# Performance work log

Hardware: AMD Instinct MI355X
Metric: run time of the kernel (lower is better)

Reference implementation:

```python
import jax, jax.numpy as jnp
import numpy as np
import math

LMAX = 3
NUM_LAYERS = 2
MUL = 32
AVG_NEIGH = 16.0
CUTOFF = 2.5
P_ENV = 6
N_RB = 8

# ---------- real Clebsch-Gordan (Wigner 3j) coefficients ----------

def _su2_cg(j1, j2, j3, m1, m2, m3):
    if m1 + m2 != m3:
        return 0.0
    f = math.factorial
    pref = math.sqrt((2 * j3 + 1) * f(j1 + j2 - j3) * f(j1 - j2 + j3) * f(-j1 + j2 + j3) / f(j1 + j2 + j3 + 1)
                     * f(j3 + m3) * f(j3 - m3) * f(j1 - m1) * f(j1 + m1) * f(j2 - m2) * f(j2 + m2))
    s = 0.0
    kmin = max(0, j2 - j3 - m1, j1 - j3 + m2)
    kmax = min(j1 + j2 - j3, j1 - m1, j2 + m2)
    for k in range(kmin, kmax + 1):
        s += (-1.0) ** k / (f(k) * f(j1 + j2 - j3 - k) * f(j1 - m1 - k) * f(j2 + m2 - k)
                            * f(j3 - j2 + m1 + k) * f(j3 - j1 - m2 + k))
    return pref * s

def _q_real_to_complex(l):
    q = np.zeros((2 * l + 1, 2 * l + 1), dtype=np.complex128)
    for m in range(-l, 0):
        q[l + m, l + abs(m)] = 1 / np.sqrt(2)
        q[l + m, l - abs(m)] = -1j / np.sqrt(2)
    q[l, l] = 1.0
    for m in range(1, l + 1):
        q[l + m, l + abs(m)] = (-1) ** m / np.sqrt(2)
        q[l + m, l - abs(m)] = 1j * (-1) ** m / np.sqrt(2)
    return (-1j) ** l * q

def _real_cg(l1, l2, l3):
    C = np.zeros((2 * l1 + 1, 2 * l2 + 1, 2 * l3 + 1), dtype=np.complex128)
    for m1 in range(-l1, l1 + 1):
        for m2 in range(-l2, l2 + 1):
            m3 = m1 + m2
            if abs(m3) <= l3:
                C[l1 + m1, l2 + m2, l3 + m3] = _su2_cg(l1, l2, l3, m1, m2, m3)
    Q1, Q2, Q3 = _q_real_to_complex(l1), _q_real_to_complex(l2), _q_real_to_complex(l3)
    C = np.einsum('ia,jb,kc,abc->ijk', Q1, Q2, np.conj(Q3), C)
    Cr, Ci = np.real(C), np.imag(C)
    C = Cr if np.linalg.norm(Cr) >= np.linalg.norm(Ci) else Ci
    return (C / np.linalg.norm(C)).astype(np.float32)  # unit-norm invariant coupling tensor

W3J = {}
for _l1 in range(LMAX + 1):
    for _l2 in range(LMAX + 1):
        for _l3 in range(LMAX + 1):
            if abs(_l1 - _l2) <= _l3 <= _l1 + _l2:
                W3J[(_l1, _l2, _l3)] = jnp.asarray(_real_cg(_l1, _l2, _l3))

# ---------- spherical harmonics (component normalization, l=0..3) ----------

def _sh(u):
    x, y, z = u[:, 0], u[:, 1], u[:, 2]
    s3, s5, s15 = math.sqrt(3.0), math.sqrt(5.0), math.sqrt(15.0)
    sh0 = jnp.ones_like(x)[:, None]
    sh1 = s3 * jnp.stack([y, z, x], -1)
    sh2 = jnp.stack([s15 * x * y, s15 * y * z, 0.5 * s5 * (3 * z * z - 1.0),
                     s15 * x * z, 0.5 * s15 * (x * x - y * y)], -1)
    c1, c2, c3, c4 = math.sqrt(35.0 / 8.0), math.sqrt(105.0), math.sqrt(21.0 / 8.0), 0.5 * math.sqrt(7.0)
    sh3 = jnp.stack([c1 * y * (3 * x * x - y * y), c2 * x * y * z, c3 * y * (5 * z * z - 1.0),
                     c4 * z * (5 * z * z - 3.0), c3 * x * (5 * z * z - 1.0),
                     0.5 * c2 * z * (x * x - y * y), c1 * x * (x * x - 3 * y * y)], -1)
    return [sh0, sh1, sh2, sh3]

def _mlp(x, Ws):
    # e3nn-style MLP: no biases, 1/sqrt(fan_in) normalization, silu, linear last layer
    for i, W in enumerate(Ws):
        x = x @ (W / jnp.sqrt(1.0 * W.shape[0]))
        if i + 1 < len(Ws):
            x = jax.nn.silu(x)
    return x

def _envelope(x):
    p = P_ENV
    e = (1.0 - 0.5 * (p + 1) * (p + 2) * x ** p + p * (p + 2) * x ** (p + 1)
         - 0.5 * p * (p + 1) * x ** (p + 2))
    return jnp.where(x < 1.0, e, 0.0)

def _forward(node_attrs, vectors, we0, we1, winit, wenv, wlat0, wlat1, wmix, wout, senders, receivers):
    N = node_attrs.shape[0]
    E = vectors.shape[0]
    d = jnp.linalg.norm(vectors, axis=-1)                      # [E]
    uvec = vectors / (d[:, None] + 1e-9)                       # unit edge vectors
    dc = d / CUTOFF                                            # normalized distance in [0, inf)
    freqs = np.pi * np.arange(1, N_RB + 1, dtype=np.float32)
    rb = math.sqrt(2.0) * jnp.sin(dc[:, None] * freqs) / (dc[:, None] + 1e-9)  # [E, 8] Bessel basis
    cut = _envelope(dc)[:, None]                               # [E, 1] polynomial cutoff u(d, p)
    # two-body embedding: radial basis + sender/receiver species
    x = jnp.concatenate([rb, node_attrs[senders], node_attrs[receivers]], axis=-1)
    x = _mlp(x, [we0, we1]) * cut                              # [E, H]
    Y = _sh(uvec)                                              # list of [E, 2l+1]
    wi = (x @ (winit / jnp.sqrt(1.0 * winit.shape[0]))).reshape(E, LMAX + 1, MUL)
    V = [wi[:, l, :, None] * Y[l][:, None, :] for l in range(LMAX + 1)]  # [E, MUL, 2l+1]
    for layer in range(NUM_LAYERS):
        w = x @ (wenv[layer] / jnp.sqrt(1.0 * wenv.shape[1]))  # [E, MUL] env weights
        env = []
        for l in range(LMAX + 1):
            # environment embedding: scatter weighted SH onto nodes, gather back onto edges
            node_env = jax.ops.segment_sum(w[:, :, None] * Y[l][:, None, :], receivers, num_segments=N)
            env.append(node_env[senders] / jnp.sqrt(AVG_NEIGH))
        # equivariant CG tensor product env (x) V -> T, per output l3
        T = []
        for l3 in range(LMAX + 1):
            acc = None
            n = 0
            for l1 in range(LMAX + 1):
                for l2 in range(LMAX + 1):
                    if (l1, l2, l3) in W3J:
                        t = jnp.einsum('ijk,emi,emj->emk', W3J[(l1, l2, l3)], env[l1], V[l2])
                        acc = t if acc is None else acc + t
                        n += 1
            T.append(acc / np.sqrt(n))
        # scalars feed the latent track; latent MLP gated by cutoff
        x = jnp.concatenate([x, T[0][:, :, 0]], axis=-1)       # [E, H+MUL]
        x = _mlp(x, [wlat0[layer], wlat1[layer]]) * cut        # [E, H]
        # per-l channel mixing (e3nn Linear)
        V = [jnp.einsum('emk,mn->enk', T[l], wmix[layer, l] / jnp.sqrt(1.0 * MUL)) for l in range(LMAX + 1)]
    # output head: 0e per-edge scalar
    return x @ (wout / jnp.sqrt(1.0 * wout.shape[0]))          # [E, 1]

def setup_inputs():
    key = jax.random.key(0)
    ks = jax.random.split(key, 12)
    N, E, S, H = 4096, 65536, 16, 512
    L = NUM_LAYERS
    return {
        'node_attrs': jax.random.normal(ks[0], (N, S), jnp.float32),
        'vectors': jax.random.normal(ks[1], (E, 3), jnp.float32),
        'we0': jax.random.normal(ks[2], (N_RB + 2 * S, H), jnp.float32),
        'we1': jax.random.normal(ks[3], (H, H), jnp.float32),
        'winit': jax.random.normal(ks[4], (H, (LMAX + 1) * MUL), jnp.float32),
        'wenv': jax.random.normal(ks[5], (L, H, MUL), jnp.float32),
        'wlat0': jax.random.normal(ks[6], (L, H + MUL, H), jnp.float32),
        'wlat1': jax.random.normal(ks[7], (L, H, H), jnp.float32),
        'wmix': jax.random.normal(ks[8], (L, LMAX + 1, MUL, MUL), jnp.float32),
        'wout': jax.random.normal(ks[9], (H, 1), jnp.float32),
        'senders': jax.random.randint(ks[10], (E,), 0, N, jnp.int32),
        'receivers': jax.random.randint(ks[11], (E,), 0, N, jnp.int32),
    }

def reference(node_attrs, vectors, we0, we1, winit, wenv, wlat0, wlat1, wmix, wout, senders, receivers):
    return _forward(node_attrs, vectors, we0, we1, winit, wenv, wlat0, wlat1, wmix, wout, senders, receivers)
```

## Files before the change

kernel.cpp:

```cpp
#include <hip/hip_runtime.h>
#include <math.h>
#include <type_traits>

typedef __attribute__((ext_vector_type(8))) short s8v;
typedef __attribute__((ext_vector_type(4))) float f4v;
typedef __attribute__((ext_vector_type(2))) float f2v;

#define CH 8192

__device__ inline float b2f(unsigned short u){ return __uint_as_float(((unsigned)u)<<16); }
__device__ inline unsigned short f2b(float f){
  unsigned u = __float_as_uint(f);
  return (unsigned short)((u + 0x7FFFu + ((u>>16)&1u)) >> 16);
}
__device__ inline void stC(float* p, float v){ *p = v; }
__device__ inline void stC(unsigned short* p, float v){ *p = f2b(v); }

__device__ __forceinline__ void gl16(const void* g, void* l){
  __builtin_amdgcn_global_load_lds(
      (const __attribute__((address_space(1))) unsigned*)g,
      (__attribute__((address_space(3))) unsigned*)l, 16, 0, 0);
}

constexpr double FCT[11] = {1.,1.,2.,6.,24.,120.,720.,5040.,40320.,362880.,3628800.};
constexpr double csqrt_c(double x){
  double g = x > 1.0 ? x : 1.0;
  for (int i=0;i<60;i++) g = 0.5*(g + x/g);
  return g;
}
struct CD { double re, im; };
constexpr CD cmulc(CD a, CD b){ return {a.re*b.re - a.im*b.im, a.re*b.im + a.im*b.re}; }

constexpr double su2cg_c(int j1,int j2,int j3,int m1,int m2,int m3){
  if (m1+m2 != m3) return 0.0;
  double pref = csqrt_c((double)(2*j3+1) * FCT[j1+j2-j3]*FCT[j1-j2+j3]*FCT[-j1+j2+j3]/FCT[j1+j2+j3+1]
              * FCT[j3+m3]*FCT[j3-m3]*FCT[j1-m1]*FCT[j1+m1]*FCT[j2-m2]*FCT[j2+m2]);
  int kmin = 0;
  if (j2-j3-m1 > kmin) kmin = j2-j3-m1;
  if (j1-j3+m2 > kmin) kmin = j1-j3+m2;
  int kmax = j1+j2-j3;
  if (j1-m1 < kmax) kmax = j1-m1;
  if (j2+m2 < kmax) kmax = j2+m2;
  double s = 0.0;
  for (int k=kmin;k<=kmax;k++){
    double t = 1.0/(FCT[k]*FCT[j1+j2-j3-k]*FCT[j1-m1-k]*FCT[j2+m2-k]*FCT[j3-j2+m1+k]*FCT[j3-j1-m2+k]);
    s += (k&1) ? -t : t;
  }
  return pref*s;
}

constexpr CD qelem_c(int l, int i, int j){
  int m = i - l;
  const double is2 = 0.70710678118654752440;
  double re=0.0, im=0.0;
  if (m < 0){
    if (j == l - m) re = is2;
    else if (j == l + m) im = -is2;
  } else if (m == 0){
    if (j == l) re = 1.0;
  } else {
    double sgn = (m & 1) ? -1.0 : 1.0;
    if (j == l + m) re = sgn*is2;
    else if (j == l - m) im = sgn*is2;
  }
  CD r{};
  switch (l & 3){
    case 0: r = {re, im}; break;
    case 1: r = {im, -re}; break;
    case 2: r = {-re, -im}; break;
    default: r = {-im, re}; break;
  }
  return r;
}

constexpr double TN3[4] = {0.5, 1.0/3.0, 0.30151134457776363, 0.31622776601683794};

template<int L1,int L2,int L3>
struct TriVals { float v[(2*L1+1)*(2*L2+1)*(2*L3+1)]; };

template<int L1,int L2,int L3>
constexpr TriVals<L1,L2,L3> make_tri(){
  constexpr int n1=2*L1+1, n2=2*L2+1, n3=2*L3+1;
  double cg[n1*n2*n3] = {};
  for (int a=0;a<n1;a++)
    for (int b=0;b<n2;b++)
      for (int c=0;c<n3;c++)
        cg[(a*n2+b)*n3+c] = su2cg_c(L1,L2,L3, a-L1, b-L2, c-L3);
  double cr[n1*n2*n3] = {};
  double ci[n1*n2*n3] = {};
  for (int i=0;i<n1;i++)
   for (int j=0;j<n2;j++)
    for (int k=0;k<n3;k++){
      double sre=0.0, sim=0.0;
      for (int a=0;a<n1;a++){
        CD q1 = qelem_c(L1,i,a);
        if (q1.re==0.0 && q1.im==0.0) continue;
        for (int b=0;b<n2;b++){
          CD q2 = qelem_c(L2,j,b);
          if (q2.re==0.0 && q2.im==0.0) continue;
          CD q12 = cmulc(q1,q2);
          for (int c=0;c<n3;c++){
            double g = cg[(a*n2+b)*n3+c];
            if (g == 0.0) continue;
            CD q3 = qelem_c(L3,k,c);
            CD q3c{q3.re, -q3.im};
            CD q = cmulc(q12,q3c);
            sre += q.re*g; sim += q.im*g;
          }
        }
      }
      cr[(i*n2+j)*n3+k]=sre; ci[(i*n2+j)*n3+k]=sim;
    }
  double nr=0.0, ni=0.0;
  for (int i=0;i<n1*n2*n3;i++){ nr += cr[i]*cr[i]; ni += ci[i]*ci[i]; }
  bool pr = nr >= ni;
  double nn = csqrt_c(pr ? nr : ni);
  TriVals<L1,L2,L3> t{};
  for (int i=0;i<n1*n2*n3;i++)
    t.v[i] = (float)(((pr ? cr[i] : ci[i]) / nn) * TN3[L3]);
  return t;
}

template<int L1,int L2,int L3>
constexpr TriVals<L1,L2,L3> W3V = make_tri<L1,L2,L3>();

constexpr int LOFFC[4] = {0,1,4,9};

template<int WB>
__device__ __forceinline__ void fmac_lit(float& a, float p){
  asm("v_fmac_f32 %0, %2, %1" : "+v"(a) : "v"(p), "i"(WB));
}

template<int I, int N, typename F>
__device__ __forceinline__ void sfor(F&& f){
  if constexpr (I < N){
    f(std::integral_constant<int,I>{});
    sfor<I+1,N>(static_cast<F&&>(f));
  }
}

template<int L1,int L2>
__device__ __forceinline__ void tp_pair(const float* __restrict__ env,
                                        const float* __restrict__ v,
                                        float* __restrict__ acc){
  sfor<0,2*L1+1>([&](auto K1c){
    constexpr int k1 = decltype(K1c)::value;
    sfor<0,2*L2+1>([&](auto K2c){
      constexpr int k2 = decltype(K2c)::value;
      float p = env[LOFFC[L1]+k1] * v[LOFFC[L2]+k2];
      sfor<0,4>([&](auto L3c){
        constexpr int l3 = decltype(L3c)::value;
        constexpr int lo = (L1>L2)?(L1-L2):(L2-L1);
        if constexpr (l3 >= lo && l3 <= L1+L2){
          sfor<0,2*l3+1>([&](auto K3c){
            constexpr int k3 = decltype(K3c)::value;
            constexpr float w = W3V<L1,L2,l3>.v[(k1*(2*L2+1)+k2)*(2*l3+1)+k3];
            if constexpr (w != 0.f){
              fmac_lit<__builtin_bit_cast(int, w)>(acc[LOFFC[l3]+k3], p);
            }
          });
        }
      });
    });
  });
}

template<int L1,int L2,int L3>
__device__ __forceinline__ void tp_tri(const float* __restrict__ env,
                                       const float* __restrict__ v,
                                       float* __restrict__ acc){
  constexpr int n1=2*L1+1, n2=2*L2+1, n3=2*L3+1;
  #pragma unroll
  for (int k1=0;k1<n1;k1++)
    #pragma unroll
    for (int k2=0;k2<n2;k2++){
      float p = env[LOFFC[L1]+k1] * v[LOFFC[L2]+k2];
      #pragma unroll
      for (int k3=0;k3<n3;k3++){
        float w = W3V<L1,L2,L3>.v[(k1*n2+k2)*n3+k3];
        if (w != 0.f) acc[LOFFC[L3]+k3] += w * p;
      }
    }
}

struct WSeg { const float* W; unsigned short* WT; int K, N, Kpad, nblk, trans; };
struct WDesc { WSeg s[11]; };
__global__ __launch_bounds__(256) void wconv_all(WDesc d){
  int b = blockIdx.x;
  int seg = 0;
  while (b >= d.s[seg].nblk){ b -= d.s[seg].nblk; ++seg; }
  const WSeg w = d.s[seg];
  int idx = b*256 + threadIdx.x;
  if (w.trans){
    if (idx >= w.N*w.Kpad) return;
    int n = idx / w.Kpad, k = idx - n*w.Kpad;
    w.WT[idx] = (k < w.K) ? f2b(w.W[(size_t)k*w.N + n]) : (unsigned short)0;
  } else {
    if (idx >= w.K*w.N) return;
    w.WT[idx] = f2b(w.W[idx]);
  }
}

__global__ __launch_bounds__(256) void edge_init(
    const float* __restrict__ vec, const float* __restrict__ na,
    const int* __restrict__ snd, const int* __restrict__ rcv,
    unsigned short* __restrict__ feat, float* __restrict__ Y, float* __restrict__ cutb,
    int* __restrict__ deg, int E)
{
  int e = blockIdx.x*256 + threadIdx.x;
  if (e >= E) return;
  float vx = vec[(size_t)e*3], vy = vec[(size_t)e*3+1], vz = vec[(size_t)e*3+2];
  float d = sqrtf(vx*vx + vy*vy + vz*vz);
  float inv = 1.f/(d + 1e-9f);
  float x = vx*inv, y = vy*inv, z = vz*inv;
  float dc = d * 0.4f;
  float dci = 1.f/(dc + 1e-9f);
  unsigned short* f = feat + (size_t)e*64;
  #pragma unroll
  for (int k=1;k<=8;k++)
    f[k-1] = f2b(1.41421356237309515f * sinf(dc * 3.14159265358979323846f * k) * dci);
  int s = snd[e], r = rcv[e];
  atomicAdd(&deg[r], 1);
  #pragma unroll
  for (int i=0;i<16;i++) f[8+i]  = f2b(na[(size_t)s*16+i]);
  #pragma unroll
  for (int i=0;i<16;i++) f[24+i] = f2b(na[(size_t)r*16+i]);
  #pragma unroll
  for (int i=40;i<64;i++) f[i] = 0;
  float cv = 0.f;
  if (dc < 1.f){
    float d2 = dc*dc; float d6 = d2*d2*d2; float d7 = d6*dc; float d8 = d7*dc;
    cv = 1.f - 28.f*d6 + 48.f*d7 - 21.f*d8;
  }
  cutb[e] = cv;
  float* Ye = Y + (size_t)e*16;
  const float s3=1.7320508075688772f, s5=2.2360679774997896f, s15=3.8729833462074170f;
  Ye[0] = 1.f;
  Ye[1] = s3*y; Ye[2] = s3*z; Ye[3] = s3*x;
  Ye[4] = s15*x*y; Ye[5] = s15*y*z; Ye[6] = 0.5f*s5*(3.f*z*z-1.f);
  Ye[7] = s15*x*z; Ye[8] = 0.5f*s15*(x*x - y*y);
  const float c1=2.0916500663351889f, c2=10.246950765959598f, c3=1.6201851746019649f, c4=1.3228756555322954f;
  Ye[9]  = c1*y*(3.f*x*x - y*y);
  Ye[10] = c2*x*y*z;
  Ye[11] = c3*y*(5.f*z*z - 1.f);
  Ye[12] = c4*z*(5.f*z*z - 3.f);
  Ye[13] = c3*x*(5.f*z*z - 1.f);
  Ye[14] = 0.5f*c2*z*(x*x - y*y);
  Ye[15] = c1*x*(x*x - 3.f*y*y);
}

template<int NT, typename TC, bool SILU, bool CUT, bool TSTORE=false>
__global__ __launch_bounds__(256) void gemm_mfma(
    const unsigned short* __restrict__ A, int lda, int K1,
    const unsigned short* __restrict__ WT, int ldw,
    TC* __restrict__ C, int ldc,
    const float* __restrict__ cutv,
    int N, int K, float scale)
{
  constexpr int NB = NT/16;
  __shared__ s8v As8[128*8];
  __shared__ s8v Bs8[NT*8];
  const int tid = threadIdx.x;
  const int wid = tid >> 6, lane = tid & 63;
  const int r15 = lane & 15, kg = lane >> 4;
  const int col0 = blockIdx.x * NT;
  const int row0 = blockIdx.y * 128;
  f4v acc[2][NB] = {};

  auto compute = [&](){
    #pragma unroll
    for (int s = 0; s < 2; s++) {
      const int cb = s*4 + kg;
      const int cx = cb ^ (r15 & 7);
      s8v a0 = As8[(wid*32      + r15)*8 + cx];
      s8v a1 = As8[(wid*32 + 16 + r15)*8 + cx];
      #pragma unroll
      for (int j = 0; j < NB; j++) {
        s8v b = Bs8[(j*16 + r15)*8 + cx];
        acc[0][j] = __builtin_amdgcn_mfma_f32_16x16x32_bf16(a0, b, acc[0][j], 0,0,0);
        acc[1][j] = __builtin_amdgcn_mfma_f32_16x16x32_bf16(a1, b, acc[1][j], 0,0,0);
      }
    }
  };

  for (int k0 = 0; k0 < K; k0 += 64) {
    #pragma unroll
    for (int i = 0; i < 4; i++) {
      int seg = i*256 + tid;
      int r = seg >> 3, ks = seg & 7;
      int ksx = ks ^ (r & 7);
      gl16(A + (size_t)(row0+r)*lda + k0 + ksx*8, &As8[i*256 + (tid & ~63)]);
    }
    #pragma unroll
    for (int i = 0; i < NT/32; i++) {
      int seg = i*256 + tid;
      int n = seg >> 3, ks = seg & 7;
      int ksx = ks ^ (n & 7);
      gl16(WT + (size_t)(col0+n)*ldw + k0 + ksx*8, &Bs8[i*256 + (tid & ~63)]);
    }
    __syncthreads();
    compute();
    __syncthreads();
  }
  #pragma unroll
  for (int g=0; g<2; g++) {
    #pragma unroll
    for (int c=0; c<NB; c++) {
      int col = col0 + c*16 + r15;
      if (col >= N) continue;
      #pragma unroll
      for (int j=0;j<4;j++) {
        int row = row0 + wid*32 + g*16 + kg*4 + j;
        float v = acc[g][c][j] * scale;
        if (SILU) v = v / (1.f + __expf(-v));
        if (CUT)  v *= cutv[row];
        if (TSTORE) stC(&C[(size_t)col*ldc + row], v);
        else        stC(&C[(size_t)row*ldc + col], v);
      }
    }
  }
}

__global__ __launch_bounds__(256) void vbuild(
    const unsigned short* __restrict__ xbc, const float* __restrict__ Y,
    unsigned short* __restrict__ V, int count)
{
  int t = blockIdx.x*256 + threadIdx.x;
  if (t >= count*32) return;
  int e = t >> 5, m = t & 31;
  const unsigned short* wr = xbc + (size_t)e*672 + 544 + m;
  float ws[4] = { b2f(wr[0]), b2f(wr[32]), b2f(wr[64]), b2f(wr[96]) };
  const float4* Y4 = (const float4*)(Y + (size_t)e*16);
  float yv[16];
  #pragma unroll
  for (int q=0;q<4;q++){ float4 f=Y4[q]; yv[q*4]=f.x; yv[q*4+1]=f.y; yv[q*4+2]=f.z; yv[q*4+3]=f.w; }
  constexpr int LOFK[16] = {0,1,1,1,2,2,2,2,2,3,3,3,3,3,3,3};
  s8v o0, o1;
  #pragma unroll
  for (int k=0;k<8;k++)  o0[k] = (short)f2b(ws[LOFK[k]]   * yv[k]);
  #pragma unroll
  for (int k=0;k<8;k++)  o1[k] = (short)f2b(ws[LOFK[8+k]] * yv[8+k]);
  s8v* vo = (s8v*)(V + (size_t)e*512 + (size_t)m*16);
  vo[0] = o0; vo[1] = o1;
}

__global__ __launch_bounds__(256) void scan_k(
    const int* __restrict__ deg, int* __restrict__ offs, int Nn)
{
  __shared__ int part[256];
  const int t = threadIdx.x;
  const int per = (Nn + 255) / 256;
  int base = t*per;
  int loc[32];
  int s = 0;
  for (int i=0;i<per;i++){ int v = (base+i<Nn)?deg[base+i]:0; loc[i]=s; s+=v; }
  part[t] = s;
  __syncthreads();
  for (int off=1; off<256; off<<=1){
    int v = (t>=off) ? part[t-off] : 0;
    __syncthreads();
    part[t] += v;
    __syncthreads();
  }
  int pre = (t==0) ? 0 : part[t-1];
  for (int i=0;i<per;i++) if (base+i<Nn) offs[base+i] = pre + loc[i];
  if (t==255) offs[Nn] = part[255];
}

__global__ __launch_bounds__(256) void fill_k(
    const int* __restrict__ rcv, int* __restrict__ cursor,
    const int* __restrict__ offs, int* __restrict__ elist, int E)
{
  int e = blockIdx.x*256 + threadIdx.x;
  if (e >= E) return;
  int r = rcv[e];
  int p = atomicAdd(&cursor[r], 1);
  elist[offs[r] + p] = e;
}

__global__ __launch_bounds__(512) void env_build(
    const unsigned short* __restrict__ xb, const float* __restrict__ Y,
    const int* __restrict__ elist, const int* __restrict__ offs,
    float* __restrict__ nenv)
{
  const int n = blockIdx.x;
  const int j = threadIdx.x;
  const int m = j >> 4, kk = j & 15;
  const int beg = offs[n], end = offs[n+1];
  float acc = 0.f;
  for (int p = beg; p < end; ++p) {
    int e = elist[p];
    acc += b2f(xb[(size_t)e*672 + 512 + m]) * Y[(size_t)e*16 + kk];
  }
  nenv[(size_t)n*512 + j] = acc;
}

__global__ __launch_bounds__(256, 2) void tp_mix(
    const float* __restrict__ nenv, const int* __restrict__ senders,
    unsigned short* __restrict__ V,
    const float* __restrict__ wm,
    unsigned short* __restrict__ xb, int E)
{
  __shared__ float Ts[8][32][18];
  const int tid = threadIdx.x;
  const int le = tid >> 5, m = tid & 31;
  const int e = blockIdx.x*8 + le;
  const int s = senders[e];
  float env[16], v[16], acc[16];
  const float4* ne4 = (const float4*)(nenv + (size_t)s*512 + (size_t)m*16);
  #pragma unroll
  for (int q=0;q<4;q++){
    float4 f = ne4[q];
    env[q*4]=f.x; env[q*4+1]=f.y; env[q*4+2]=f.z; env[q*4+3]=f.w;
  }
  const s8v* vv = (const s8v*)(V + (size_t)e*512 + (size_t)m*16);
  s8v v0 = vv[0], v1 = vv[1];
  #pragma unroll
  for (int q=0;q<8;q++){ v[q] = b2f((unsigned short)v0[q]); v[8+q] = b2f((unsigned short)v1[q]); }
  #pragma unroll
  for (int k=0;k<16;k++) acc[k] = 0.f;

  tp_pair<0,0>(env,v,acc); tp_pair<0,1>(env,v,acc); tp_pair<0,2>(env,v,acc); tp_pair<0,3>(env,v,acc);
  tp_pair<1,0>(env,v,acc); tp_pair<1,1>(env,v,acc); tp_pair<1,2>(env,v,acc); tp_pair<1,3>(env,v,acc);
  tp_pair<2,0>(env,v,acc); tp_pair<2,1>(env,v,acc); tp_pair<2,2>(env,v,acc); tp_pair<2,3>(env,v,acc);
  tp_pair<3,0>(env,v,acc); tp_pair<3,1>(env,v,acc); tp_pair<3,2>(env,v,acc); tp_pair<3,3>(env,v,acc);

  xb[(size_t)e*672 + 512 + m] = f2b(acc[0]);

  #pragma unroll
  for (int k=0;k<16;k++) Ts[le][m][k] = acc[k];
  f2v o2[8];
  #pragma unroll
  for (int kp=0;kp<8;kp++){ o2[kp][0]=0.f; o2[kp][1]=0.f; }
  #pragma unroll
  for (int mm=0; mm<32; mm++) {
    float w0 = wm[        mm*32 + m];
    float w1 = wm[1024 +  mm*32 + m];
    float w2 = wm[2048 +  mm*32 + m];
    float w3 = wm[3072 +  mm*32 + m];
    const f2v* tr = (const f2v*)Ts[le][mm];
    f2v p01; p01[0]=w0; p01[1]=w1;
    f2v p11; p11[0]=w1; p11[1]=w1;
    f2v p22; p22[0]=w2; p22[1]=w2;
    f2v p23; p23[0]=w2; p23[1]=w3;
    f2v p33; p33[0]=w3; p33[1]=w3;
    o2[0] += tr[0]*p01; o2[1] += tr[1]*p11; o2[2] += tr[2]*p22; o2[3] += tr[3]*p22;
    o2[4] += tr[4]*p23; o2[5] += tr[5]*p33; o2[6] += tr[6]*p33; o2[7] += tr[7]*p33;
  }
  s8v oa, ob;
  #pragma unroll
  for (int kp=0;kp<4;kp++){
    oa[2*kp]   = (short)f2b(o2[kp][0]   * 0.17677669529663689f);
    oa[2*kp+1] = (short)f2b(o2[kp][1]   * 0.17677669529663689f);
    ob[2*kp]   = (short)f2b(o2[4+kp][0] * 0.17677669529663689f);
    ob[2*kp+1] = (short)f2b(o2[4+kp][1] * 0.17677669529663689f);
  }
  s8v* vo = (s8v*)(V + (size_t)e*512 + (size_t)m*16);
  vo[0] = oa; vo[1] = ob;
}

__global__ __launch_bounds__(256) void tp_last(
    const float* __restrict__ nenv, const int* __restrict__ senders,
    const unsigned short* __restrict__ V, unsigned short* __restrict__ xb, int E)
{
  int t = blockIdx.x*256 + threadIdx.x;
  int e = t >> 5, m = t & 31;
  if (e >= E) return;
  int s = senders[e];
  float env[16], v[16], acc[16];
  const float4* ne4 = (const float4*)(nenv + (size_t)s*512 + (size_t)m*16);
  #pragma unroll
  for (int q=0;q<4;q++){
    float4 f = ne4[q];
    env[q*4]=f.x; env[q*4+1]=f.y; env[q*4+2]=f.z; env[q*4+3]=f.w;
  }
  const s8v* vv = (const s8v*)(V + (size_t)e*512 + (size_t)m*16);
  s8v v0 = vv[0], v1 = vv[1];
  #pragma unroll
  for (int q=0;q<8;q++){ v[q] = b2f((unsigned short)v0[q]); v[8+q] = b2f((unsigned short)v1[q]); }
  #pragma unroll
  for (int k=0;k<16;k++) acc[k] = 0.f;
  tp_tri<0,0,0>(env,v,acc); tp_tri<1,1,0>(env,v,acc);
  tp_tri<2,2,0>(env,v,acc); tp_tri<3,3,0>(env,v,acc);
  xb[(size_t)e*672 + 512 + m] = f2b(acc[0]);
}

__global__ __launch_bounds__(256) void out_kernel(
    const unsigned short* __restrict__ x, const float* __restrict__ wout,
    float* __restrict__ out, int E)
{
  int gw = (blockIdx.x*256 + threadIdx.x) >> 6;
  int lane = threadIdx.x & 63;
  if (gw >= E) return;
  const s8v* xr = (const s8v*)(x + (size_t)gw*672);
  s8v chunk = xr[lane];
  float s = 0.f;
  #pragma unroll
  for (int j=0;j<8;j++) s += b2f((unsigned short)chunk[j]) * wout[lane*8 + j];
  #pragma unroll
  for (int off=32; off; off>>=1) s += __shfl_down(s, off);
  if (lane == 0) out[gw] = s * 0.044194173824159216f;
}

static inline size_t alup(size_t b){ return (b + 255) & ~(size_t)255; }
static size_t need_bytes(int E, int N, int chd){
  size_t s = 0;
  s += alup((size_t)E*16*4);
  s += alup((size_t)E*4);
  s += alup((size_t)N*512*4);
  s += alup((size_t)E*64*2);
  s += alup((size_t)chd*512*2);
  s += alup((size_t)E*512*2);
  s += alup((size_t)E*672*2);
  s += alup((size_t)512*64*2);
  s += alup((size_t)768*512*2);
  s += alup((size_t)128*512*2);
  s += alup((size_t)2*32*512*2);
  s += alup((size_t)2*512*576*2);
  s += alup((size_t)640*512*2);
  s += alup((size_t)512*512*2);
  s += alup((size_t)512*512*2);
  s += alup((size_t)512*512*2);
  s += alup((size_t)N*4);
  s += alup(((size_t)N+1)*4);
  s += alup((size_t)N*4);
  s += alup((size_t)E*4);
  return s;
}

extern "C" void kernel_launch(void* const* d_in, const int* in_sizes, int n_in,
                              void* d_out, int out_size, void* d_ws, size_t ws_size,
                              hipStream_t stream)
{
  const float* node_attrs = (const float*)d_in[0];
  const float* vectors    = (const float*)d_in[1];
  const float* we0        = (const float*)d_in[2];
  const float* we1        = (const float*)d_in[3];
  const float* winit      = (const float*)d_in[4];
  const float* wenv       = (const float*)d_in[5];
  const float* wlat0      = (const float*)d_in[6];
  const float* wlat1      = (const float*)d_in[7];
  const float* wmix       = (const float*)d_in[8];
  const float* wout       = (const float*)d_in[9];
  const int*   senders    = (const int*)d_in[10];
  const int*   receivers  = (const int*)d_in[11];
  float* out = (float*)d_out;
  const int E = in_sizes[1] / 3;
  const int N = in_sizes[0] / 16;

  int CHD = -1;
  const int tiers[4] = {E, E/2, E/4, CH};
  for (int i=0;i<4;i++){
    if (tiers[i] >= CH && need_bytes(E, N, tiers[i]) <= ws_size){ CHD = tiers[i]; break; }
  }
  if (CHD < 0) return;

  char* base = (char*)d_ws;
  size_t off = 0;
  auto carve = [&](size_t b) -> char* { char* p = base + off; off += alup(b); return p; };
  float*          Yb    = (float*)carve((size_t)E*16*4);
  float*          cutb  = (float*)carve((size_t)E*4);
  float*          nenv  = (float*)carve((size_t)N*512*4);
  unsigned short* feat  = (unsigned short*)carve((size_t)E*64*2);
  unsigned short* cbuf  = (unsigned short*)carve((size_t)CHD*512*2);
  unsigned short* Vb    = (unsigned short*)carve((size_t)E*512*2);
  unsigned short* xb    = (unsigned short*)carve((size_t)E*672*2);
  unsigned short* we0T  = (unsigned short*)carve((size_t)512*64*2);
  unsigned short* weF   = (unsigned short*)carve((size_t)768*512*2);
  unsigned short* winT  = (unsigned short*)carve((size_t)128*512*2);
  unsigned short* wenvT = (unsigned short*)carve((size_t)2*32*512*2);
  unsigned short* wl0T  = (unsigned short*)carve((size_t)2*512*576*2);
  unsigned short* wl1F  = (unsigned short*)carve((size_t)640*512*2);
  unsigned short* wl1T1 = (unsigned short*)carve((size_t)512*512*2);
  unsigned short* we1c  = (unsigned short*)carve((size_t)512*512*2);
  unsigned short* wl1c  = (unsigned short*)carve((size_t)512*512*2);
  int*            deg   = (int*)carve((size_t)N*4);
  int*            offs  = (int*)carve(((size_t)N+1)*4);
  int*            cursor= (int*)carve((size_t)N*4);
  int*            elist = (int*)carve((size_t)E*4);

  const float rs40  = 0.15811388300841897f;
  const float rs512 = 0.044194173824159216f;
  const float rs544 = 0.042874646285627205f;

  dim3 blk(256);
  hipMemsetAsync(deg, 0, (size_t)N*4, stream);
  hipMemsetAsync(cursor, 0, (size_t)N*4, stream);

  WDesc wd;
  auto seg = [&](int i, const float* W, unsigned short* WT, int K, int Nn, int Kpad, int trans){
    int elems = trans ? Nn*Kpad : K*Nn;
    wd.s[i] = { W, WT, K, Nn, Kpad, (elems + 255)/256, trans };
  };
  seg(0, we0,   we0T, 40, 512, 64, 1);
  seg(1, we1,   weF,  512, 512, 512, 1);
  seg(2, winit, winT, 512, 128, 512, 1);
  seg(3, wenv,                  wenvT,                  512, 32, 512, 1);
  seg(4, wenv + (size_t)512*32, wenvT + (size_t)32*512, 512, 32, 512, 1);
  seg(5, wlat0,                   wl0T,                   544, 512, 576, 1);
  seg(6, wlat0 + (size_t)544*512, wl0T + (size_t)512*576, 544, 512, 576, 1);
  seg(7, wlat1,                   wl1F,  512, 512, 512, 1);
  seg(8, wlat1 + (size_t)512*512, wl1T1, 512, 512, 512, 1);
  seg(9, we1,   we1c, 512, 512, 512, 0);
  seg(10, wlat1, wl1c, 512, 512, 512, 0);
  int totblk = 0;
  for (int i=0;i<11;i++) totblk += wd.s[i].nblk;
  wconv_all<<<totblk, blk, 0, stream>>>(wd);

  gemm_mfma<64,unsigned short,false,false,true><<<dim3(1,4), blk, 0, stream>>>(
      we1c, 512, 512, wenvT, 512, weF + (size_t)512*512, 512, nullptr, 32, 512, rs512*0.25f);
  gemm_mfma<128,unsigned short,false,false,true><<<dim3(1,4), blk, 0, stream>>>(
      we1c, 512, 512, winT, 512, weF + (size_t)544*512, 512, nullptr, 128, 512, rs512);
  gemm_mfma<64,unsigned short,false,false,true><<<dim3(1,4), blk, 0, stream>>>(
      wl1c, 512, 512, wenvT + (size_t)32*512, 512, wl1F + (size_t)512*512, 512, nullptr, 32, 512, rs512*0.25f);

  edge_init<<<E/256, blk, 0, stream>>>(vectors, node_attrs, senders, receivers, feat, Yb, cutb, deg, E);

  scan_k<<<1, blk, 0, stream>>>(deg, offs, N);
  fill_k<<<(E+255)/256, blk, 0, stream>>>(receivers, cursor, offs, elist, E);

  for (int c0 = 0; c0 < E; c0 += CHD) {
    gemm_mfma<128,unsigned short,true,false><<<dim3(4, CHD/128), blk, 0, stream>>>(
        feat + (size_t)c0*64, 64, 64, we0T, 64, cbuf, 512, nullptr, 512, 64, rs40);
    gemm_mfma<128,unsigned short,false,true><<<dim3(6, CHD/128), blk, 0, stream>>>(
        cbuf, 512, 512, weF, 512, xb + (size_t)c0*672, 672, cutb + c0, 672, 512, rs512);
    vbuild<<<(CHD*32)/256, blk, 0, stream>>>(xb + (size_t)c0*672, Yb + (size_t)c0*16, Vb + (size_t)c0*512, CHD);
  }

  for (int layer = 0; layer < 2; ++layer) {
    env_build<<<N, 512, 0, stream>>>(xb, Yb, elist, offs, nenv);
    if (layer == 0)
      tp_mix<<<E/8, blk, 0, stream>>>(nenv, senders, Vb,
          wmix, xb, E);
    else
      tp_last<<<(E*32)/256, blk, 0, stream>>>(nenv, senders, Vb, xb, E);
    for (int c0 = 0; c0 < E; c0 += CHD) {
      gemm_mfma<128,unsigned short,true,false><<<dim3(4, CHD/128), blk, 0, stream>>>(
          xb + (size_t)c0*672, 672, 576, wl0T + (size_t)layer*512*576, 576,
          cbuf, 512, nullptr, 512, 576, rs544);
      if (layer == 0)
        gemm_mfma<128,unsigned short,false,true><<<dim3(5, CHD/128), blk, 0, stream>>>(
            cbuf, 512, 512, wl1F, 512, xb + (size_t)c0*672, 672, cutb + c0, 544, 512, rs512);
      else
        gemm_mfma<128,unsigned short,false,true><<<dim3(4, CHD/128), blk, 0, stream>>>(
            cbuf, 512, 512, wl1T1, 512, xb + (size_t)c0*672, 672, cutb + c0, 512, 512, rs512);
    }
  }

  out_kernel<<<E/4, blk, 0, stream>>>(xb, wout, out, E);
}
```

Measured before the change: 679.2 us.

## Fold last-layer linear and output projection into a single precomputed vector

Because the last layer's second linear is followed directly by a linear readout, this multiplies wlat1[1] by wout once up front to get a 512-vector. The final 512x512 GEMM per chunk is then replaced by a per-edge dot product on the intermediate activations, scaled by the cutoff. This removes a large GEMM and the separate output pass. The catch is that it only holds if no nonlinearity sits after that GEMM, and it changes where bf16 rounding happens.

After: 633.8 us (median of 2 runs). 6.7% less time.

```diff
diff --git a/kernel.cpp b/kernel.cpp
--- a/kernel.cpp
+++ b/kernel.cpp
@@ -184,7 +184,7 @@
 }
 
 struct WSeg { const float* W; unsigned short* WT; int K, N, Kpad, nblk, trans; };
-struct WDesc { WSeg s[11]; };
+struct WDesc { WSeg s[10]; };
 __global__ __launch_bounds__(256) void wconv_all(WDesc d){
   int b = blockIdx.x;
   int seg = 0;
@@ -199,6 +199,17 @@
     if (idx >= w.K*w.N) return;
     w.WT[idx] = f2b(w.W[idx]);
   }
+}
+
+__global__ __launch_bounds__(256) void wfuse_vec(
+    const float* __restrict__ wl1_l1, const float* __restrict__ wout,
+    float* __restrict__ fv)
+{
+  int k = blockIdx.x*256 + threadIdx.x;
+  if (k >= 512) return;
+  float s = 0.f;
+  for (int n=0;n<512;n++) s += wl1_l1[(size_t)k*512 + n] * wout[n];
+  fv[k] = s;
 }
 
 __global__ __launch_bounds__(256) void edge_init(
@@ -485,21 +496,22 @@
   xb[(size_t)e*672 + 512 + m] = f2b(acc[0]);
 }
 
-__global__ __launch_bounds__(256) void out_kernel(
-    const unsigned short* __restrict__ x, const float* __restrict__ wout,
-    float* __restrict__ out, int E)
+__global__ __launch_bounds__(256) void out_fused(
+    const unsigned short* __restrict__ h, const float* __restrict__ fv,
+    const float* __restrict__ cutv, float* __restrict__ out, int count)
 {
   int gw = (blockIdx.x*256 + threadIdx.x) >> 6;
   int lane = threadIdx.x & 63;
-  if (gw >= E) return;
-  const s8v* xr = (const s8v*)(x + (size_t)gw*672);
+  if (gw >= count) return;
+  const s8v* xr = (const s8v*)(h + (size_t)gw*512);
   s8v chunk = xr[lane];
   float s = 0.f;
   #pragma unroll
-  for (int j=0;j<8;j++) s += b2f((unsigned short)chunk[j]) * wout[lane*8 + j];
+  for (int j=0;j<8;j++) s += b2f((unsigned short)chunk[j]) * fv[lane*8 + j];
   #pragma unroll
   for (int off=32; off; off>>=1) s += __shfl_down(s, off);
-  if (lane == 0) out[gw] = s * 0.044194173824159216f;
+  if (lane == 0)
+    out[gw] = s * cutv[gw] * (0.044194173824159216f * 0.044194173824159216f);
 }
 
 static inline size_t alup(size_t b){ return (b + 255) & ~(size_t)255; }
@@ -520,7 +532,7 @@
   s += alup((size_t)640*512*2);
   s += alup((size_t)512*512*2);
   s += alup((size_t)512*512*2);
-  s += alup((size_t)512*512*2);
+  s += alup(512*4);
   s += alup((size_t)N*4);
   s += alup(((size_t)N+1)*4);
   s += alup((size_t)N*4);
@@ -571,9 +583,9 @@
   unsigned short* wenvT = (unsigned short*)carve((size_t)2*32*512*2);
   unsigned short* wl0T  = (unsigned short*)carve((size_t)2*512*576*2);
   unsigned short* wl1F  = (unsigned short*)carve((size_t)640*512*2);
-  unsigned short* wl1T1 = (unsigned short*)carve((size_t)512*512*2);
   unsigned short* we1c  = (unsigned short*)carve((size_t)512*512*2);
   unsigned short* wl1c  = (unsigned short*)carve((size_t)512*512*2);
+  float*          fv    = (float*)carve(512*4);
   int*            deg   = (int*)carve((size_t)N*4);
   int*            offs  = (int*)carve(((size_t)N+1)*4);
   int*            cursor= (int*)carve((size_t)N*4);
@@ -600,12 +612,12 @@
   seg(5, wlat0,                   wl0T,                   544, 512, 576, 1);
   seg(6, wlat0 + (size_t)544*512, wl0T + (size_t)512*576, 544, 512, 576, 1);
   seg(7, wlat1,                   wl1F,  512, 512, 512, 1);
-  seg(8, wlat1 + (size_t)512*512, wl1T1, 512, 512, 512, 1);
-  seg(9, we1,   we1c, 512, 512, 512, 0);
-  seg(10, wlat1, wl1c, 512, 512, 512, 0);
+  seg(8, we1,   we1c, 512, 512, 512, 0);
+  seg(9, wlat1, wl1c, 512, 512, 512, 0);
   int totblk = 0;
-  for (int i=0;i<11;i++) totblk += wd.s[i].nblk;
+  for (int i=0;i<10;i++) totblk += wd.s[i].nblk;
   wconv_all<<<totblk, blk, 0, stream>>>(wd);
+  wfuse_vec<<<2, blk, 0, stream>>>(wlat1 + (size_t)512*512, wout, fv);
 
   gemm_mfma<64,unsigned short,false,false,true><<<dim3(1,4), blk, 0, stream>>>(
       we1c, 512, 512, wenvT, 512, weF + (size_t)512*512, 512, nullptr, 32, 512, rs512*0.25f);
@@ -642,10 +654,7 @@
         gemm_mfma<128,unsigned short,false,true><<<dim3(5, CHD/128), blk, 0, stream>>>(
             cbuf, 512, 512, wl1F, 512, xb + (size_t)c0*672, 672, cutb + c0, 544, 512, rs512);
       else
-        gemm_mfma<128,unsigned short,false,true><<<dim3(4, CHD/128), blk, 0, stream>>>(
-            cbuf, 512, 512, wl1T1, 512, xb + (size_t)c0*672, 672, cutb + c0, 512, 512, rs512);
+        out_fused<<<CHD/4, blk, 0, stream>>>(cbuf, fv, cutb + c0, out + c0, CHD);
     }
   }
-
-  out_kernel<<<E/4, blk, 0, stream>>>(xb, wout, out, E);
-}
+}
```
